# Kernel optimization log

Hardware: AMD Instinct MI355X
Metric: run time of the kernel (lower is better)

The kernel has to match this reference:

```python
import jax, jax.numpy as jnp
import numpy as np

N = 100000
E = 1600000
IN_C = 512
OUT_C = 128


def setup_inputs() -> dict:
    key = jax.random.key(0)
    k1, k2, k3, k4 = jax.random.split(key, 4)
    x = jax.random.normal(k1, (N, IN_C), dtype=jnp.float32)
    edge_index = jax.random.randint(k2, (2, E), 0, N, dtype=jnp.int64)
    # GCNConv parameters (glorot weight, zero bias as in PyG defaults)
    scale = jnp.sqrt(6.0 / (IN_C + OUT_C)).astype(jnp.float32)
    W = jax.random.uniform(k3, (IN_C, OUT_C), dtype=jnp.float32, minval=-scale, maxval=scale)
    b = jnp.zeros((OUT_C,), dtype=jnp.float32)
    return {"x": x, "edge_index": edge_index, "W": W, "b": b}


def reference(x, edge_index, W, b):
    n = x.shape[0]
    loops = jnp.arange(n, dtype=edge_index.dtype)
    src = jnp.concatenate([edge_index[0], loops])  # [E+N] message sources
    dst = jnp.concatenate([edge_index[1], loops])  # [E+N] message targets
    # symmetric GCN normalization: deg over targets incl. self-loops
    deg = jax.ops.segment_sum(jnp.ones_like(src, dtype=x.dtype), dst, num_segments=n)
    dinv = jnp.where(deg > 0, jax.lax.rsqrt(deg), 0.0)
    norm = dinv[src] * dinv[dst]  # [E+N]
    h = x @ W  # [N, OUT_C] transform first (in > out)
    msg = h[src] * norm[:, None]  # [E+N, OUT_C]
    out = jax.ops.segment_sum(msg, dst, num_segments=n) + b
    return (out, 0)
```

## Files before the change

### kernel.cpp

```cpp
#include <hip/hip_runtime.h>

#define IN_C 512
#define OUT_C 128
#define NB 128
#define CHUNK 8192

typedef float f32x4 __attribute__((ext_vector_type(4)));
typedef __bf16 bf16x8 __attribute__((ext_vector_type(8)));

static inline int cdiv(int a, int b) { return (a + b - 1) / b; }

__device__ __forceinline__ unsigned short bfbits(__bf16 h) {
  return __builtin_bit_cast(unsigned short, h);
}


__global__ __launch_bounds__(256) void hist_kernel(const int* __restrict__ dst,
                                                   int* __restrict__ table,
                                                   int nchunks, int E) {
  __shared__ int hcnt[NB];
  int t = threadIdx.x;
  int c = blockIdx.x;
  if (t < NB) hcnt[t] = 0;
  __syncthreads();
  int base = c * CHUNK;
  for (int i = t; i < CHUNK; i += 256) {
    int e = base + i;
    if (e < E) atomicAdd(&hcnt[dst[e] >> 10], 1);
  }
  __syncthreads();
  if (t < NB) table[t * nchunks + c] = hcnt[t];
}

__global__ __launch_bounds__(256) void tscan_kernel(int* __restrict__ table,
                                                    int* __restrict__ bstart,
                                                    int nchunks, int E) {
  __shared__ int sh[256];
  int t = threadIdx.x;
  int total = NB * nchunks;
  int S = (total + 255) / 256;
  int lo = t * S;
  int hi = lo + S; if (hi > total) hi = total;
  int s = 0;
  int i = lo;
  for (; i + 4 <= hi; i += 4)
    s += table[i] + table[i + 1] + table[i + 2] + table[i + 3];
  for (; i < hi; i++) s += table[i];
  sh[t] = s;
  __syncthreads();
  for (int off = 1; off < 256; off <<= 1) {
    int x = sh[t];
    if (t >= off) x += sh[t - off];
    __syncthreads();
    sh[t] = x;
    __syncthreads();
  }
  int run = sh[t] - s;
  for (i = lo; i < hi; i++) {
    int v = table[i];
    table[i] = run;
    run += v;
  }
  __syncthreads();
  for (int b = t; b < NB; b += 256) bstart[b] = table[b * nchunks];
  if (t == 0) bstart[NB] = E;
}

__global__ __launch_bounds__(256) void scat2_kernel(const int* __restrict__ src,
                                                    const int* __restrict__ dst,
                                                    const int* __restrict__ table,
                                                    int* __restrict__ inter,
                                                    int nchunks, int E) {
  __shared__ int cur[NB];
  int t = threadIdx.x;
  int c = blockIdx.x;
  if (t < NB) cur[t] = table[t * nchunks + c];
  __syncthreads();
  int base = c * CHUNK;
  for (int i = t; i < CHUNK; i += 256) {
    int e = base + i;
    if (e < E) {
      int d = dst[e];
      int pos = atomicAdd(&cur[d >> 10], 1);
      inter[pos] = (src[e] << 10) | (d & 1023);
    }
  }
}

__global__ __launch_bounds__(256) void bucket_csr_kernel(const int* __restrict__ inter,
                                                         const int* __restrict__ bstart,
                                                         int* __restrict__ offs,
                                                         float* __restrict__ dinv,
                                                         int* __restrict__ csr_src,
                                                         int n, int E, int nbk) {
  __shared__ int dl[1024];
  __shared__ int curs[1024];
  __shared__ int sh[256];
  int t = threadIdx.x;
  int b = blockIdx.x;
  for (int i = t; i < 1024; i += 256) dl[i] = 0;
  __syncthreads();
  int lo = bstart[b], hi = bstart[b + 1];
  for (int e = lo + t; e < hi; e += 256) atomicAdd(&dl[inter[e] & 1023], 1);
  __syncthreads();
  int c[4];
  int s = 0;
#pragma unroll
  for (int j = 0; j < 4; j++) {
    c[j] = dl[t * 4 + j];
    s += c[j];
  }
  sh[t] = s;
  __syncthreads();
  for (int off = 1; off < 256; off <<= 1) {
    int x = sh[t];
    if (t >= off) x += sh[t - off];
    __syncthreads();
    sh[t] = x;
    __syncthreads();
  }
  int run = sh[t] - s + lo;
  int nb0 = b << 10;
#pragma unroll
  for (int j = 0; j < 4; j++) {
    int node = nb0 + t * 4 + j;
    if (node < n) {
      offs[node] = run;
      dinv[node] = rsqrtf((float)c[j] + 1.0f);
    }
    curs[t * 4 + j] = run;
    run += c[j];
  }
  if (b == nbk - 1 && t == 255) offs[n] = E;
  __syncthreads();
  for (int e = lo + t; e < hi; e += 256) {
    int u = inter[e];
    int pos = atomicAdd(&curs[u & 1023], 1);
    csr_src[pos] = u >> 10;
  }
}

__global__ __launch_bounds__(256) void wsplit_kernel(const float* __restrict__ W,
                                                     unsigned short* __restrict__ wfh,
                                                     unsigned short* __restrict__ wfl) {
  int i = blockIdx.x * 256 + threadIdx.x;
  if (i >= IN_C * OUT_C) return;
  int k = i >> 7;
  int col = i & 127;
  float w = W[i];
  __bf16 hb = (__bf16)w;
  __bf16 lb = (__bf16)(w - (float)hb);
  int ks = k >> 5;
  int lg = (k & 31) >> 3;
  int j = k & 7;
  int cb = col >> 4;
  int lane = lg * 16 + (col & 15);
  size_t idx = ((size_t)(ks * 8 + cb) * 64 + lane) * 8 + j;
  wfh[idx] = bfbits(hb);
  wfl[idx] = bfbits(lb);
}

__global__ __launch_bounds__(256) void gemm_mfma_kernel(
    const float* __restrict__ x, const unsigned short* __restrict__ wfh,
    const unsigned short* __restrict__ wfl, const float* __restrict__ dinv,
    unsigned short* __restrict__ h, int n) {
  __shared__ float xs[2][4096];

  const int tid = threadIdx.x;
  const int wv = tid >> 6;
  const int lane = tid & 63;
  const int l15 = lane & 15;
  const int lg = lane >> 4;
  const int wr = wv >> 1;
  const int wc = wv & 1;
  const int row0 = blockIdx.x * 128;

  const float* gsrc[4];
#pragma unroll
  for (int i = 0; i < 4; i++) {
    int pslot = i * 256 + tid;
    int row = pslot >> 3;
    int q = pslot & 7;
    int s = q ^ (row & 7);
    int grow = row0 + row;
    if (grow > n - 1) grow = n - 1;
    gsrc[i] = x + (size_t)grow * IN_C + s * 4;
  }

  const unsigned short* bph = wfh + ((size_t)(wc * 4) * 64 + lane) * 8;
  const unsigned short* bpl = wfl + ((size_t)(wc * 4) * 64 + lane) * 8;

  f32x4 acc[4][4];
#pragma unroll
  for (int i = 0; i < 4; i++)
#pragma unroll
    for (int j = 0; j < 4; j++) acc[i][j] = (f32x4)0.0f;

#pragma unroll
  for (int i = 0; i < 4; i++) {
    char* lp = (char*)&xs[0][0] + i * 4096 + wv * 1024;
    __builtin_amdgcn_global_load_lds(
        (const __attribute__((address_space(1))) void*)gsrc[i],
        (__attribute__((address_space(3))) void*)lp, 16, 0, 0);
    gsrc[i] += 32;
  }
  __syncthreads();

  int cur = 0;
  for (int ks = 0; ks < 16; ks++) {
    if (ks < 15) {
#pragma unroll
      for (int i = 0; i < 4; i++) {
        char* lp = (char*)&xs[cur ^ 1][0] + i * 4096 + wv * 1024;
        __builtin_amdgcn_global_load_lds(
            (const __attribute__((address_space(1))) void*)gsrc[i],
            (__attribute__((address_space(3))) void*)lp, 16, 0, 0);
        gsrc[i] += 32;
      }
    }
    bf16x8 bh[4], bl[4];
#pragma unroll
    for (int nt = 0; nt < 4; nt++) {
      bh[nt] = __builtin_bit_cast(bf16x8, *(const uint4*)(bph + (size_t)ks * 4096 + nt * 512));
      bl[nt] = __builtin_bit_cast(bf16x8, *(const uint4*)(bpl + (size_t)ks * 4096 + nt * 512));
    }
    const float* bp = &xs[cur][0];
    bf16x8 ah[4];
#pragma unroll
    for (int rt = 0; rt < 4; rt++) {
      int row = wr * 64 + rt * 16 + l15;
      int r7 = row & 7;
      int s0 = (lg * 2) ^ r7;
      int s1 = (lg * 2 + 1) ^ r7;
      float4 f0 = *(const float4*)(bp + row * 32 + s0 * 4);
      float4 f1 = *(const float4*)(bp + row * 32 + s1 * 4);
      float f[8] = {f0.x, f0.y, f0.z, f0.w, f1.x, f1.y, f1.z, f1.w};
      bf16x8 hh;
#pragma unroll
      for (int j = 0; j < 8; j++) hh[j] = (__bf16)f[j];
      ah[rt] = hh;
    }
#pragma unroll
    for (int rt = 0; rt < 4; rt++)
#pragma unroll
      for (int nt = 0; nt < 4; nt++) {
        acc[rt][nt] = __builtin_amdgcn_mfma_f32_16x16x32_bf16(ah[rt], bh[nt], acc[rt][nt], 0, 0, 0);
        acc[rt][nt] = __builtin_amdgcn_mfma_f32_16x16x32_bf16(ah[rt], bl[nt], acc[rt][nt], 0, 0, 0);
      }
    __syncthreads();
    cur ^= 1;
  }

#pragma unroll
  for (int rt = 0; rt < 4; rt++) {
    int rowbase = row0 + wr * 64 + rt * 16 + lg * 4;
#pragma unroll
    for (int r = 0; r < 4; r++) {
      int row = rowbase + r;
      if (row < n) {
        float di = dinv[row];
#pragma unroll
        for (int nt = 0; nt < 4; nt++) {
          int col = wc * 64 + nt * 16 + l15;
          h[(size_t)row * OUT_C + col] = bfbits((__bf16)(acc[rt][nt][r] * di));
        }
      }
    }
  }
}

__device__ __forceinline__ float bflo(unsigned int u) {
  return __builtin_bit_cast(float, u << 16);
}
__device__ __forceinline__ float bfhi(unsigned int u) {
  return __builtin_bit_cast(float, u & 0xffff0000u);
}

__global__ __launch_bounds__(256) void gather_kernel(const int* __restrict__ offs,
                                                     const int* __restrict__ csr_src,
                                                     const unsigned short* __restrict__ h,
                                                     const float* __restrict__ dinv,
                                                     const float* __restrict__ b,
                                                     float* __restrict__ out,
                                                     int n, int tail) {
  int wid = threadIdx.x >> 6;
  int lane = threadIdx.x & 63;
  int l15 = lane & 15;
  int q = lane >> 4;
  int node = blockIdx.x * 4 + wid;
  if (node >= n) return;

  int start = offs[node];
  int end = offs[node + 1];

  float ax0 = 0, ay0 = 0, ax1 = 0, ay1 = 0, ax2 = 0, ay2 = 0, ax3 = 0, ay3 = 0;

  int e = start + q;
  for (; e + 12 < end; e += 16) {
    int s0 = csr_src[e];
    int s1 = csr_src[e + 4];
    int s2 = csr_src[e + 8];
    int s3 = csr_src[e + 12];
    uint4 u0 = *(const uint4*)(h + (size_t)s0 * OUT_C + l15 * 8);
    uint4 u1 = *(const uint4*)(h + (size_t)s1 * OUT_C + l15 * 8);
    uint4 u2 = *(const uint4*)(h + (size_t)s2 * OUT_C + l15 * 8);
    uint4 u3 = *(const uint4*)(h + (size_t)s3 * OUT_C + l15 * 8);
    ax0 += (bflo(u0.x) + bflo(u1.x)) + (bflo(u2.x) + bflo(u3.x));
    ay0 += (bfhi(u0.x) + bfhi(u1.x)) + (bfhi(u2.x) + bfhi(u3.x));
    ax1 += (bflo(u0.y) + bflo(u1.y)) + (bflo(u2.y) + bflo(u3.y));
    ay1 += (bfhi(u0.y) + bfhi(u1.y)) + (bfhi(u2.y) + bfhi(u3.y));
    ax2 += (bflo(u0.z) + bflo(u1.z)) + (bflo(u2.z) + bflo(u3.z));
    ay2 += (bfhi(u0.z) + bfhi(u1.z)) + (bfhi(u2.z) + bfhi(u3.z));
    ax3 += (bflo(u0.w) + bflo(u1.w)) + (bflo(u2.w) + bflo(u3.w));
    ay3 += (bfhi(u0.w) + bfhi(u1.w)) + (bfhi(u2.w) + bfhi(u3.w));
  }
  for (; e < end; e += 4) {
    int s0 = csr_src[e];
    uint4 u0 = *(const uint4*)(h + (size_t)s0 * OUT_C + l15 * 8);
    ax0 += bflo(u0.x); ay0 += bfhi(u0.x);
    ax1 += bflo(u0.y); ay1 += bfhi(u0.y);
    ax2 += bflo(u0.z); ay2 += bfhi(u0.z);
    ax3 += bflo(u0.w); ay3 += bfhi(u0.w);
  }

#pragma unroll
  for (int mask = 16; mask <= 32; mask <<= 1) {
    ax0 += __shfl_xor(ax0, mask); ay0 += __shfl_xor(ay0, mask);
    ax1 += __shfl_xor(ax1, mask); ay1 += __shfl_xor(ay1, mask);
    ax2 += __shfl_xor(ax2, mask); ay2 += __shfl_xor(ay2, mask);
    ax3 += __shfl_xor(ax3, mask); ay3 += __shfl_xor(ay3, mask);
  }

  float dd = dinv[node];
  uint4 us = *(const uint4*)(h + (size_t)node * OUT_C + l15 * 8);
  ax0 = (ax0 + bflo(us.x)) * dd; ay0 = (ay0 + bfhi(us.x)) * dd;
  ax1 = (ax1 + bflo(us.y)) * dd; ay1 = (ay1 + bfhi(us.y)) * dd;
  ax2 = (ax2 + bflo(us.z)) * dd; ay2 = (ay2 + bfhi(us.z)) * dd;
  ax3 = (ax3 + bflo(us.w)) * dd; ay3 = (ay3 + bfhi(us.w)) * dd;

  if (q == 0) {
    float4 b0 = *(const float4*)(b + l15 * 8);
    float4 b1 = *(const float4*)(b + l15 * 8 + 4);
    float4 o0 = make_float4(ax0 + b0.x, ay0 + b0.y, ax1 + b0.z, ay1 + b0.w);
    float4 o1 = make_float4(ax2 + b1.x, ay2 + b1.y, ax3 + b1.z, ay3 + b1.w);
    float* op = out + (size_t)node * OUT_C + l15 * 8;
    *(float4*)op = o0;
    *(float4*)(op + 4) = o1;
  }

  if (node == 0 && lane == 0) {
    for (int t = 0; t < tail; t++) out[(size_t)n * OUT_C + t] = 0.0f;
  }
}

extern "C" void kernel_launch(void* const* d_in, const int* in_sizes, int n_in,
                              void* d_out, int out_size, void* d_ws, size_t ws_size,
                              hipStream_t stream) {
  const float* x = (const float*)d_in[0];
  const int* ei = (const int*)d_in[1];
  const float* W = (const float*)d_in[2];
  const float* b = (const float*)d_in[3];

  const int n = in_sizes[0] / IN_C;
  const int E = in_sizes[1] / 2;
  const int* src = ei;
  const int* dst = ei + E;
  float* out = (float*)d_out;

  const int nchunks = cdiv(E, CHUNK);
  const int nbk = cdiv(n, 1024);

  size_t p = 0;
  auto alloc = [&](size_t bytes) { size_t o = p; p += (bytes + 255) & ~(size_t)255; return o; };
  char* ws = (char*)d_ws;
  float*          dinv   = (float*)(ws + alloc((size_t)n * 4));
  int*            offs   = (int*)(ws + alloc(((size_t)n + 1) * 4));
  int*            csrsrc = (int*)(ws + alloc((size_t)E * 4));
  int*            bstart = (int*)(ws + alloc((NB + 1) * 4));
  unsigned short* wfh    = (unsigned short*)(ws + alloc((size_t)IN_C * OUT_C * 2));
  unsigned short* wfl    = (unsigned short*)(ws + alloc((size_t)IN_C * OUT_C * 2));
  size_t upos = p;
  int*            inter  = (int*)(ws + upos);
  int*            table  = (int*)(ws + upos + (((size_t)E * 4 + 255) & ~(size_t)255));
  unsigned short* h      = (unsigned short*)(ws + upos);

  wsplit_kernel<<<cdiv(IN_C * OUT_C, 256), 256, 0, stream>>>(W, wfh, wfl);
  hist_kernel<<<nchunks, 256, 0, stream>>>(dst, table, nchunks, E);
  tscan_kernel<<<1, 256, 0, stream>>>(table, bstart, nchunks, E);
  scat2_kernel<<<nchunks, 256, 0, stream>>>(src, dst, table, inter, nchunks, E);
  bucket_csr_kernel<<<nbk, 256, 0, stream>>>(inter, bstart, offs, dinv, csrsrc, n, E, nbk);
  gemm_mfma_kernel<<<cdiv(n, 128), 256, 0, stream>>>(x, wfh, wfl, dinv, h, n);
  int tail = out_size - n * OUT_C;
  gather_kernel<<<cdiv(n, 4), 256, 0, stream>>>(offs, csrsrc, h, dinv, b, out, n, tail);
}
```

Before: 264.7 us.

## Fold weight split into histogram kernel and compute per-node degrees with global atomics

Merges the weight bf16 hi/lo split into extra blocks of the histogram launch, which removes one kernel launch. The histogram pass also counts per-node in-degree with global atomics, so the bucket CSR kernel can read degrees directly instead of running its own shared-memory counting pass over the bucketed edges. The chunk size is reduced to produce more blocks. The cost is 1.6M global atomics, heavily contended and scattered, plus a memset of the degree array.

```diff
diff --git a/kernel.cpp b/kernel.cpp
--- a/kernel.cpp
+++ b/kernel.cpp
@@ -3,7 +3,7 @@
 #define IN_C 512
 #define OUT_C 128
 #define NB 128
-#define CHUNK 8192
+#define CHUNK 6144
 
 typedef float f32x4 __attribute__((ext_vector_type(4)));
 typedef __bf16 bf16x8 __attribute__((ext_vector_type(8)));
@@ -17,16 +17,41 @@
 
 __global__ __launch_bounds__(256) void hist_kernel(const int* __restrict__ dst,
                                                    int* __restrict__ table,
+                                                   int* __restrict__ deg,
+                                                   const float* __restrict__ W,
+                                                   unsigned short* __restrict__ wfh,
+                                                   unsigned short* __restrict__ wfl,
                                                    int nchunks, int E) {
+  int c = blockIdx.x;
+  int t = threadIdx.x;
+  if (c >= nchunks) {
+    int i = (c - nchunks) * 256 + t;
+    if (i < IN_C * OUT_C) {
+      int k = i >> 7;
+      int col = i & 127;
+      float w = W[i];
+      __bf16 hb = (__bf16)w;
+      __bf16 lb = (__bf16)(w - (float)hb);
+      int ks = k >> 5;
+      int lg = (k & 31) >> 3;
+      int j = k & 7;
+      int cb = col >> 4;
+      int lane = lg * 16 + (col & 15);
+      size_t idx = ((size_t)(ks * 8 + cb) * 64 + lane) * 8 + j;
+      wfh[idx] = bfbits(hb);
+      wfl[idx] = bfbits(lb);
+    }
+    return;
+  }
   __shared__ int hcnt[NB];
-  int t = threadIdx.x;
-  int c = blockIdx.x;
   if (t < NB) hcnt[t] = 0;
   __syncthreads();
   int base = c * CHUNK;
-  for (int i = t; i < CHUNK; i += 256) {
-    int e = base + i;
-    if (e < E) atomicAdd(&hcnt[dst[e] >> 10], 1);
+  int lim = base + CHUNK < E ? base + CHUNK : E;
+  for (int e = base + t; e < lim; e += 256) {
+    int d = dst[e];
+    atomicAdd(&hcnt[d >> 10], 1);
+    atomicAdd(&deg[d], 1);
   }
   __syncthreads();
   if (t < NB) table[t * nchunks + c] = hcnt[t];
@@ -77,39 +102,37 @@
   if (t < NB) cur[t] = table[t * nchunks + c];
   __syncthreads();
   int base = c * CHUNK;
-  for (int i = t; i < CHUNK; i += 256) {
-    int e = base + i;
-    if (e < E) {
-      int d = dst[e];
-      int pos = atomicAdd(&cur[d >> 10], 1);
-      inter[pos] = (src[e] << 10) | (d & 1023);
-    }
+  int lim = base + CHUNK < E ? base + CHUNK : E;
+  for (int e = base + t; e < lim; e += 256) {
+    int d = dst[e];
+    int pos = atomicAdd(&cur[d >> 10], 1);
+    inter[pos] = (src[e] << 10) | (d & 1023);
   }
 }
 
 __global__ __launch_bounds__(256) void bucket_csr_kernel(const int* __restrict__ inter,
                                                          const int* __restrict__ bstart,
+                                                         const int* __restrict__ deg,
                                                          int* __restrict__ offs,
                                                          float* __restrict__ dinv,
                                                          int* __restrict__ csr_src,
                                                          int n, int E, int nbk) {
-  __shared__ int dl[1024];
   __shared__ int curs[1024];
   __shared__ int sh[256];
   int t = threadIdx.x;
   int b = blockIdx.x;
-  for (int i = t; i < 1024; i += 256) dl[i] = 0;
-  __syncthreads();
   int lo = bstart[b], hi = bstart[b + 1];
-  for (int e = lo + t; e < hi; e += 256) atomicAdd(&dl[inter[e] & 1023], 1);
-  __syncthreads();
+  int nb0 = b << 10;
+  int base = nb0 + t * 4;
   int c[4];
-  int s = 0;
-#pragma unroll
-  for (int j = 0; j < 4; j++) {
-    c[j] = dl[t * 4 + j];
-    s += c[j];
-  }
+  if (base + 3 < n) {
+    int4 v = *(const int4*)(deg + base);
+    c[0] = v.x; c[1] = v.y; c[2] = v.z; c[3] = v.w;
+  } else {
+#pragma unroll
+    for (int j = 0; j < 4; j++) c[j] = (base + j < n) ? deg[base + j] : 0;
+  }
+  int s = c[0] + c[1] + c[2] + c[3];
   sh[t] = s;
   __syncthreads();
   for (int off = 1; off < 256; off <<= 1) {
@@ -120,10 +143,9 @@
     __syncthreads();
   }
   int run = sh[t] - s + lo;
-  int nb0 = b << 10;
 #pragma unroll
   for (int j = 0; j < 4; j++) {
-    int node = nb0 + t * 4 + j;
+    int node = base + j;
     if (node < n) {
       offs[node] = run;
       dinv[node] = rsqrtf((float)c[j] + 1.0f);
@@ -138,26 +160,6 @@
     int pos = atomicAdd(&curs[u & 1023], 1);
     csr_src[pos] = u >> 10;
   }
-}
-
-__global__ __launch_bounds__(256) void wsplit_kernel(const float* __restrict__ W,
-                                                     unsigned short* __restrict__ wfh,
-                                                     unsigned short* __restrict__ wfl) {
-  int i = blockIdx.x * 256 + threadIdx.x;
-  if (i >= IN_C * OUT_C) return;
-  int k = i >> 7;
-  int col = i & 127;
-  float w = W[i];
-  __bf16 hb = (__bf16)w;
-  __bf16 lb = (__bf16)(w - (float)hb);
-  int ks = k >> 5;
-  int lg = (k & 31) >> 3;
-  int j = k & 7;
-  int cb = col >> 4;
-  int lane = lg * 16 + (col & 15);
-  size_t idx = ((size_t)(ks * 8 + cb) * 64 + lane) * 8 + j;
-  wfh[idx] = bfbits(hb);
-  wfl[idx] = bfbits(lb);
 }
 
 __global__ __launch_bounds__(256) void gemm_mfma_kernel(
@@ -376,6 +378,7 @@
   float*          dinv   = (float*)(ws + alloc((size_t)n * 4));
   int*            offs   = (int*)(ws + alloc(((size_t)n + 1) * 4));
   int*            csrsrc = (int*)(ws + alloc((size_t)E * 4));
+  int*            deg    = (int*)(ws + alloc((size_t)n * 4));
   int*            bstart = (int*)(ws + alloc((NB + 1) * 4));
   unsigned short* wfh    = (unsigned short*)(ws + alloc((size_t)IN_C * OUT_C * 2));
   unsigned short* wfl    = (unsigned short*)(ws + alloc((size_t)IN_C * OUT_C * 2));
@@ -384,11 +387,11 @@
   int*            table  = (int*)(ws + upos + (((size_t)E * 4 + 255) & ~(size_t)255));
   unsigned short* h      = (unsigned short*)(ws + upos);
 
-  wsplit_kernel<<<cdiv(IN_C * OUT_C, 256), 256, 0, stream>>>(W, wfh, wfl);
-  hist_kernel<<<nchunks, 256, 0, stream>>>(dst, table, nchunks, E);
+  hipMemsetAsync(deg, 0, (size_t)n * 4, stream);
+  hist_kernel<<<nchunks + 256, 256, 0, stream>>>(dst, table, deg, W, wfh, wfl, nchunks, E);
   tscan_kernel<<<1, 256, 0, stream>>>(table, bstart, nchunks, E);
   scat2_kernel<<<nchunks, 256, 0, stream>>>(src, dst, table, inter, nchunks, E);
-  bucket_csr_kernel<<<nbk, 256, 0, stream>>>(inter, bstart, offs, dinv, csrsrc, n, E, nbk);
+  bucket_csr_kernel<<<nbk, 256, 0, stream>>>(inter, bstart, deg, offs, dinv, csrsrc, n, E, nbk);
   gemm_mfma_kernel<<<cdiv(n, 128), 256, 0, stream>>>(x, wfh, wfl, dinv, h, n);
   int tail = out_size - n * OUT_C;
   gather_kernel<<<cdiv(n, 4), 256, 0, stream>>>(offs, csrsrc, h, dinv, b, out, n, tail);
```

Measured after the change: 313.1 us. 1.18x slower.
